# Performance work log

Hardware: AMD Instinct MI355X
Metric: run time of the kernel (lower is better)

## Reference

```python
import jax, jax.numpy as jnp
import numpy as np

BETA = 0.25
N_E = 1024
E_DIM = 64
B, L = 32, 2048


def setup_inputs() -> dict:
    key = jax.random.key(0)
    k1, k2 = jax.random.split(key)
    z = jax.random.normal(k1, (B, L, E_DIM), dtype=jnp.float32)
    # torch init: uniform_(-1/n_e, 1/n_e)
    codebook = jax.random.uniform(k2, (N_E, E_DIM), dtype=jnp.float32,
                                  minval=-1.0 / N_E, maxval=1.0 / N_E)
    return {"z": z, "codebook": codebook}


def reference(z, codebook):
    sg = jax.lax.stop_gradient
    n_e = codebook.shape[0]
    zf = z.reshape(-1, codebook.shape[1])  # (N, e_dim)
    # squared-distance matrix: ||z||^2 + ||e||^2 - 2 z.e  -> (N, n_e)
    d = (jnp.sum(zf * zf, axis=1, keepdims=True)
         + jnp.sum(codebook * codebook, axis=1)
         - 2.0 * zf @ codebook.T)
    idx = jnp.argmin(d, axis=1)  # (N,)
    # one-hot @ codebook is just a gather
    z_q = codebook[idx].reshape(z.shape)
    loss = (jnp.mean((sg(z_q) - z) ** 2)
            + BETA * jnp.mean((z_q - sg(z)) ** 2))
    # straight-through estimator
    z_q_st = z + sg(z_q - z)
    # codebook usage stats (mean of one-hot rows == normalized histogram)
    counts = jnp.zeros((n_e,), dtype=z.dtype).at[idx].add(1.0)
    e_mean = counts / idx.shape[0]
    perplexity = jnp.exp(-jnp.sum(e_mean * jnp.log(e_mean + 1e-10)))
    return loss, z_q_st, perplexity, idx
```

## Files before the change

### kernel.cpp

```cpp
#include <hip/hip_runtime.h>
#include <math.h>

#define E_DIM 64
#define N_E   1024
#define BETA  0.25

using bf16x8 = __attribute__((ext_vector_type(8))) short;
using f32x4  = __attribute__((ext_vector_type(4))) float;
#define MFMA(a, b, c) __builtin_amdgcn_mfma_f32_16x16x32_bf16((a), (b), (c), 0, 0, 0)

#define GLOAD_LDS(g, l) __builtin_amdgcn_global_load_lds(                      \
    (const __attribute__((address_space(1))) void*)(g),                        \
    (__attribute__((address_space(3))) void*)(l), 16, 0, 0)


__device__ __forceinline__ unsigned short f2bf_rn(float f) {
    unsigned u = __builtin_bit_cast(unsigned, f);
    unsigned r = u + 0x7fffu + ((u >> 16) & 1u);
    return (unsigned short)(r >> 16);
}
__device__ __forceinline__ float bf2f(unsigned short b) {
    unsigned u = ((unsigned)b) << 16;
    return __builtin_bit_cast(float, u);
}

__device__ __forceinline__ float pw64_sq(const float* v) {
    float r[8];
#pragma unroll
    for (int l = 0; l < 8; ++l) r[l] = v[l] * v[l];
#pragma unroll
    for (int t = 1; t < 8; ++t)
#pragma unroll
        for (int l = 0; l < 8; ++l) r[l] += v[8 * t + l] * v[8 * t + l];
    return ((r[0] + r[1]) + (r[2] + r[3])) + ((r[4] + r[5]) + (r[6] + r[7]));
}

__global__ __launch_bounds__(256) void k_h(const float* __restrict__ cb,
                                           float* __restrict__ h) {
    int j = blockIdx.x * 256 + threadIdx.x;
    if (j < N_E) {
        float e[E_DIM];
        const float4* ep = reinterpret_cast<const float4*>(cb + (size_t)j * E_DIM);
#pragma unroll
        for (int k4 = 0; k4 < E_DIM / 4; ++k4) {
            float4 v = ep[k4];
            e[4 * k4 + 0] = v.x; e[4 * k4 + 1] = v.y;
            e[4 * k4 + 2] = v.z; e[4 * k4 + 3] = v.w;
        }
        h[j] = pw64_sq(e);
    }
}

__global__ __launch_bounds__(256) void k_prep(const float* __restrict__ cb,
                                              unsigned short* __restrict__ ebh,
                                              unsigned short* __restrict__ ebl) {
    int t = blockIdx.x * 256 + threadIdx.x;
    int e = t & 7, lane = (t >> 3) & 63, ks = (t >> 9) & 1, ct = t >> 10;
    int j = ct * 16 + (lane & 15);
    int k = ks * 32 + ((lane >> 4) << 3) + e;
    float v = cb[j * 64 + k];
    unsigned short hi = f2bf_rn(v);
    ebh[t] = hi;
    ebl[t] = f2bf_rn(v - bf2f(hi));
}

__global__ __launch_bounds__(256, 2) void k_mfma(
    const float* __restrict__ z, const float* __restrict__ cb,
    const float* __restrict__ h,
    const unsigned short* __restrict__ ebh, const unsigned short* __restrict__ ebl,
    float* __restrict__ out_zq, float* __restrict__ out_idx,
    unsigned* __restrict__ hist, double* __restrict__ sse,
    unsigned* __restrict__ flagN, unsigned* __restrict__ flagL) {
    const int lane = threadIdx.x & 63;
    const int w = __builtin_amdgcn_readfirstlane(threadIdx.x >> 6);
    const int m = lane & 15, g = lane >> 4;

    __shared__ __align__(16) unsigned char sB[2][2][16384];
    __shared__ int bok;
    __shared__ float rsv[4][32];
    __shared__ float sb0[4][32], sb1[4][32];
    __shared__ int   sbi[4][32];
    if (threadIdx.x == 0) bok = 1;
    __syncthreads();

    {
        bf16x8 a, b;
#pragma unroll
        for (int e = 0; e < 8; ++e) {
            int k = g * 8 + e;
            a[e] = (short)f2bf_rn((float)(((m * 3 + k * 7) & 15) - 7));
            b[e] = (short)f2bf_rn((float)(((k * 5 + m * 3) & 15) - 8));
        }
        f32x4 acc = {0.f, 0.f, 0.f, 0.f};
        acc = MFMA(a, b, acc);
        bool ok = true;
#pragma unroll
        for (int r = 0; r < 4; ++r) {
            int rw = g * 4 + r;
            float E = 0.f;
            for (int k = 0; k < 32; ++k)
                E += (float)((((rw * 3 + k * 7) & 15) - 7) * (((k * 5 + m * 3) & 15) - 8));
            ok = ok && (acc[r] == E);
        }
        if (!ok) atomicAnd(&bok, 0);
    }
    __syncthreads();
    if (!bok) {
        if (threadIdx.x < 128) {
            unsigned p = atomicAdd(flagN, 1u);
            flagL[p] = (unsigned)(blockIdx.x * 128 + threadIdx.x);
        }
        return;
    }

    const int rowb32 = blockIdx.x * 128 + w * 32;
    bf16x8 a0h0, a0l0, a0h1, a0l1, a1h0, a1l0, a1h1, a1l1;
#define ALOAD(P, AH0, AL0, AH1, AL1) {                                         \
        const int rowA = rowb32 + (P) * 16 + m;                                \
        const float4* zr = reinterpret_cast<const float4*>(z + (size_t)rowA * 64); \
        float4 p0 = zr[g * 2], p1 = zr[g * 2 + 1];                             \
        float4 p2 = zr[8 + g * 2], p3 = zr[9 + g * 2];                         \
        float t0[8] = {p0.x, p0.y, p0.z, p0.w, p1.x, p1.y, p1.z, p1.w};        \
        float t1[8] = {p2.x, p2.y, p2.z, p2.w, p3.x, p3.y, p3.z, p3.w};        \
        float s = 0.f;                                                         \
        _Pragma("unroll")                                                      \
        for (int e = 0; e < 8; ++e) {                                          \
            s += fabsf(t0[e]) + fabsf(t1[e]);                                  \
            float x0 = 2.0f * t0[e]; unsigned short h0 = f2bf_rn(x0);          \
            AH0[e] = (short)h0; AL0[e] = (short)f2bf_rn(x0 - bf2f(h0));        \
            float x1 = 2.0f * t1[e]; unsigned short h1 = f2bf_rn(x1);          \
            AH1[e] = (short)h1; AL1[e] = (short)f2bf_rn(x1 - bf2f(h1));        \
        }                                                                      \
        s += __shfl_xor(s, 16);                                                \
        s += __shfl_xor(s, 32);                                                \
        if (g == 0) rsv[w][(P) * 16 + m] = s;                                  \
    }
    ALOAD(0, a0h0, a0l0, a0h1, a0l1)
    ALOAD(1, a1h0, a1l0, a1h1, a1l1)
#undef ALOAD

#define STAGE(c, buf) {                                                        \
        const unsigned char* gh = (const unsigned char*)ebh +                  \
            (size_t)(c) * 16384 + w * 4096 + lane * 16;                        \
        const unsigned char* gl = (const unsigned char*)ebl +                  \
            (size_t)(c) * 16384 + w * 4096 + lane * 16;                        \
        unsigned char* dh = &sB[buf][0][w * 4096];                             \
        unsigned char* dl = &sB[buf][1][w * 4096];                             \
        _Pragma("unroll")                                                      \
        for (int u = 0; u < 4; ++u) {                                          \
            GLOAD_LDS(gh + u * 1024, dh + u * 1024);                           \
            GLOAD_LDS(gl + u * 1024, dl + u * 1024);                           \
        }                                                                      \
    }

    float bb00 = INFINITY, bb01 = INFINITY, bb02 = INFINITY, bb03 = INFINITY;
    float bb10 = INFINITY, bb11 = INFINITY, bb12 = INFINITY, bb13 = INFINITY;
    float ss00 = INFINITY, ss01 = INFINITY, ss02 = INFINITY, ss03 = INFINITY;
    float ss10 = INFINITY, ss11 = INFINITY, ss12 = INFINITY, ss13 = INFINITY;
    int   ii00 = 0, ii01 = 0, ii02 = 0, ii03 = 0;
    int   ii10 = 0, ii11 = 0, ii12 = 0, ii13 = 0;
#define UPD(S, B0, B1, I0) { float _s = (S);                                   \
        if (_s < B0) { B1 = B0; B0 = _s; I0 = j; } else B1 = fminf(B1, _s); }

    STAGE(0, 0);
    __syncthreads();
#pragma unroll 1
    for (int c = 0; c < 8; ++c) {
        if (c + 1 < 8) STAGE(c + 1, (c + 1) & 1);
        const bf16x8* sBh = reinterpret_cast<const bf16x8*>(&sB[c & 1][0][0]);
        const bf16x8* sBl = reinterpret_cast<const bf16x8*>(&sB[c & 1][1][0]);
#pragma unroll
        for (int ct8 = 0; ct8 < 8; ++ct8) {
            const int fb = ct8 * 128 + lane;
            bf16x8 vbh0 = sBh[fb], vbh1 = sBh[fb + 64];
            bf16x8 vbl0 = sBl[fb], vbl1 = sBl[fb + 64];
            const f32x4 z4 = {0.f, 0.f, 0.f, 0.f};
            f32x4 c0a = MFMA(a0h0, vbh0, z4);
            f32x4 c0b = MFMA(a0h1, vbh1, z4);
            f32x4 c1a = MFMA(a1h0, vbh0, z4);
            f32x4 c1b = MFMA(a1h1, vbh1, z4);
            f32x4 c0c = MFMA(a0h0, vbl0, z4);
            f32x4 c0d = MFMA(a0h1, vbl1, z4);
            f32x4 c1c = MFMA(a1h0, vbl0, z4);
            f32x4 c1d = MFMA(a1h1, vbl1, z4);
            f32x4 c0e = MFMA(a0l0, vbh0, z4);
            f32x4 c0f = MFMA(a0l1, vbh1, z4);
            f32x4 c1e = MFMA(a1l0, vbh0, z4);
            f32x4 c1f = MFMA(a1l1, vbh1, z4);
            f32x4 s0 = (c0a + c0b) + ((c0c + c0d) + (c0e + c0f));
            f32x4 s1 = (c1a + c1b) + ((c1c + c1d) + (c1e + c1f));
            const int j = (c * 8 + ct8) * 16 + m;
            const float hj = h[j];
            UPD(hj - s0[0], bb00, ss00, ii00)
            UPD(hj - s0[1], bb01, ss01, ii01)
            UPD(hj - s0[2], bb02, ss02, ii02)
            UPD(hj - s0[3], bb03, ss03, ii03)
            UPD(hj - s1[0], bb10, ss10, ii10)
            UPD(hj - s1[1], bb11, ss11, ii11)
            UPD(hj - s1[2], bb12, ss12, ii12)
            UPD(hj - s1[3], bb13, ss13, ii13)
        }
        __syncthreads();
    }
#undef STAGE
#undef UPD

#pragma unroll
    for (int mask = 1; mask < 16; mask <<= 1) {
#define MRG(B0, I0, B1) { float ob0 = __shfl_xor(B0, mask); int oi = __shfl_xor(I0, mask); \
        float ob1 = __shfl_xor(B1, mask); \
        if (ob0 < B0) { B1 = fminf(fminf(B0, B1), ob1); B0 = ob0; I0 = oi; } \
        else { B1 = fminf(B1, fminf(ob0, ob1)); } }
        MRG(bb00, ii00, ss00) MRG(bb01, ii01, ss01)
        MRG(bb02, ii02, ss02) MRG(bb03, ii03, ss03)
        MRG(bb10, ii10, ss10) MRG(bb11, ii11, ss11)
        MRG(bb12, ii12, ss12) MRG(bb13, ii13, ss13)
#undef MRG
    }

    if (m == 0) {
        sb0[w][g * 4 + 0] = bb00; sb1[w][g * 4 + 0] = ss00; sbi[w][g * 4 + 0] = ii00;
        sb0[w][g * 4 + 1] = bb01; sb1[w][g * 4 + 1] = ss01; sbi[w][g * 4 + 1] = ii01;
        sb0[w][g * 4 + 2] = bb02; sb1[w][g * 4 + 2] = ss02; sbi[w][g * 4 + 2] = ii02;
        sb0[w][g * 4 + 3] = bb03; sb1[w][g * 4 + 3] = ss03; sbi[w][g * 4 + 3] = ii03;
        sb0[w][16 + g * 4 + 0] = bb10; sb1[w][16 + g * 4 + 0] = ss10; sbi[w][16 + g * 4 + 0] = ii10;
        sb0[w][16 + g * 4 + 1] = bb11; sb1[w][16 + g * 4 + 1] = ss11; sbi[w][16 + g * 4 + 1] = ii11;
        sb0[w][16 + g * 4 + 2] = bb12; sb1[w][16 + g * 4 + 2] = ss12; sbi[w][16 + g * 4 + 2] = ii12;
        sb0[w][16 + g * 4 + 3] = bb13; sb1[w][16 + g * 4 + 3] = ss13; sbi[w][16 + g * 4 + 3] = ii13;
    }
    __syncthreads();

    {
        const int rloc = lane >> 1, q = lane & 1;
        const int rowO = rowb32 + rloc;
        const float vb0 = sb0[w][rloc];
        const float vb1 = sb1[w][rloc];
        const int   vi  = sbi[w][rloc];
        const float Delta = 6e-8f * rsv[w][rloc] + 2.2e-5f;
        float local = 0.f;
        if (vb1 - vb0 <= Delta) {
            if (q == 0) { unsigned p = atomicAdd(flagN, 1u); flagL[p] = (unsigned)rowO; }
        } else {
            if (q == 0) { out_idx[rowO] = (float)vi; atomicAdd(&hist[vi], 1u); }
            const float4* cv = reinterpret_cast<const float4*>(cb + (size_t)vi * 64) + q * 8;
            const float4* zv = reinterpret_cast<const float4*>(z + (size_t)rowO * 64) + q * 8;
            float* orow = out_zq + (size_t)rowO * 64 + q * 32;
#pragma unroll
            for (int u = 0; u < 8; ++u) {
                float4 cc = cv[u], zo = zv[u];
                orow[4 * u + 0] = cc.x; orow[4 * u + 1] = cc.y;
                orow[4 * u + 2] = cc.z; orow[4 * u + 3] = cc.w;
                float dx = cc.x - zo.x, dy = cc.y - zo.y;
                float dz = cc.z - zo.z, dw = cc.w - zo.w;
                local = fmaf(dx, dx, local); local = fmaf(dy, dy, local);
                local = fmaf(dz, dz, local); local = fmaf(dw, dw, local);
            }
        }
#pragma unroll
        for (int off = 32; off; off >>= 1) local += __shfl_down(local, off);
        if (lane == 0) atomicAdd(sse, (double)local);
    }
}

__global__ __launch_bounds__(64, 4) void k_cleanup(
    const float* __restrict__ z, const float* __restrict__ cb,
    const float* __restrict__ h,
    const unsigned* __restrict__ flagN, const unsigned* __restrict__ flagL,
    float* __restrict__ out_zq, float* __restrict__ out_idx,
    unsigned* __restrict__ hist, double* __restrict__ sse) {
    const unsigned n = *flagN;
    const int lane = threadIdx.x;

    for (unsigned f = blockIdx.x; f < n; f += gridDim.x) {
        const int row = (int)flagL[f];

        float tz[E_DIM];
        const float4* zp = reinterpret_cast<const float4*>(z + (size_t)row * 64);
#pragma unroll
        for (int k4 = 0; k4 < 16; ++k4) {
            float4 v = zp[k4];
            tz[4 * k4 + 0] = v.x; tz[4 * k4 + 1] = v.y;
            tz[4 * k4 + 2] = v.z; tz[4 * k4 + 3] = v.w;
        }
        const float nz = pw64_sq(tz);
#pragma unroll
        for (int k = 0; k < 64; ++k) tz[k] = 2.0f * tz[k];

        float bs = INFINITY;
        int bj = 0;
#pragma unroll 2
        for (int t = 0; t < 16; ++t) {
            const int j = lane + 64 * t;
            const float4* cv = reinterpret_cast<const float4*>(cb + (size_t)j * 64);
            float mm = 0.f;
#pragma unroll
            for (int k4 = 0; k4 < 16; ++k4) {
                float4 e = cv[k4];
                mm = fmaf(tz[4 * k4 + 0], e.x, mm);
                mm = fmaf(tz[4 * k4 + 1], e.y, mm);
                mm = fmaf(tz[4 * k4 + 2], e.z, mm);
                mm = fmaf(tz[4 * k4 + 3], e.w, mm);
            }
            float s = (nz + h[j]) - mm;
            if (s < bs) { bs = s; bj = j; }
        }
#pragma unroll
        for (int off = 32; off; off >>= 1) {
            float s2 = __shfl_down(bs, off);
            int   j2 = __shfl_down(bj, off);
            if (s2 < bs || (s2 == bs && j2 < bj)) { bs = s2; bj = j2; }
        }
        bj = __shfl(bj, 0);

        float c = cb[(size_t)bj * 64 + lane];
        out_zq[(size_t)row * 64 + lane] = c;
        float d = c - 0.5f * tz[lane];
        float l2 = d * d;
#pragma unroll
        for (int off = 32; off; off >>= 1) l2 += __shfl_down(l2, off);
        if (lane == 0) {
            out_idx[row] = (float)bj;
            atomicAdd(&hist[bj], 1u);
            atomicAdd(sse, (double)l2);
        }
    }
}

__global__ __launch_bounds__(512, 2) void k_scan_fb(
    const float* __restrict__ z, const float* __restrict__ cb,
    const float* __restrict__ h,
    float* __restrict__ out_zq, float* __restrict__ out_idx,
    unsigned* __restrict__ hist, double* __restrict__ sse) {
    const int lane = threadIdx.x & 63;
    const int w = __builtin_amdgcn_readfirstlane(threadIdx.x >> 6);
    const int row = blockIdx.x * 64 + lane;
    float tz[E_DIM];
    const float4* zp = reinterpret_cast<const float4*>(z + (size_t)row * E_DIM);
#pragma unroll
    for (int k4 = 0; k4 < E_DIM / 4; ++k4) {
        float4 v = zp[k4];
        tz[4 * k4 + 0] = v.x; tz[4 * k4 + 1] = v.y;
        tz[4 * k4 + 2] = v.z; tz[4 * k4 + 3] = v.w;
    }
    const float nz = pw64_sq(tz);
#pragma unroll
    for (int k = 0; k < E_DIM; ++k) tz[k] = 2.0f * tz[k];
    float b0 = INFINITY; int bi = 0;
    const int j0 = w * 128;
#pragma unroll 1
    for (int j = j0; j < j0 + 128; j += 4) {
        const float* c0 = cb + (size_t)j * E_DIM;
        float m0 = 0.f, m1 = 0.f, m2 = 0.f, m3 = 0.f;
#pragma unroll
        for (int k = 0; k < E_DIM; ++k) {
            float wk = tz[k];
            m0 = fmaf(wk, c0[0 * E_DIM + k], m0);
            m1 = fmaf(wk, c0[1 * E_DIM + k], m1);
            m2 = fmaf(wk, c0[2 * E_DIM + k], m2);
            m3 = fmaf(wk, c0[3 * E_DIM + k], m3);
        }
        float s0 = (nz + h[j + 0]) - m0;
        float s1 = (nz + h[j + 1]) - m1;
        float s2 = (nz + h[j + 2]) - m2;
        float s3 = (nz + h[j + 3]) - m3;
        if (s0 < b0) { b0 = s0; bi = j + 0; }
        if (s1 < b0) { b0 = s1; bi = j + 1; }
        if (s2 < b0) { b0 = s2; bi = j + 2; }
        if (s3 < b0) { b0 = s3; bi = j + 3; }
    }
    __shared__ float lb[8][64];
    __shared__ int   li[8][64];
    lb[w][lane] = b0; li[w][lane] = bi;
    __syncthreads();
    if (threadIdx.x < 64) {
        float b = lb[0][lane]; int i = li[0][lane];
#pragma unroll
        for (int c = 1; c < 8; ++c) {
            float bc = lb[c][lane]; int ic = li[c][lane];
            if (bc < b) { b = bc; i = ic; }
        }
        out_idx[row] = (float)i;
        float local = 0.f;
        const float4* cv = reinterpret_cast<const float4*>(cb + (size_t)i * E_DIM);
        float* orow = out_zq + (size_t)row * E_DIM;
#pragma unroll
        for (int k4 = 0; k4 < E_DIM / 4; ++k4) {
            float4 c = cv[k4];
            float zx = 0.5f * tz[4 * k4 + 0], zy = 0.5f * tz[4 * k4 + 1];
            float zz = 0.5f * tz[4 * k4 + 2], zw = 0.5f * tz[4 * k4 + 3];
            orow[4 * k4 + 0] = c.x; orow[4 * k4 + 1] = c.y;
            orow[4 * k4 + 2] = c.z; orow[4 * k4 + 3] = c.w;
            float dx = c.x - zx, dy = c.y - zy, dz = c.z - zz, dw = c.w - zw;
            local = fmaf(dx, dx, local); local = fmaf(dy, dy, local);
            local = fmaf(dz, dz, local); local = fmaf(dw, dw, local);
        }
        atomicAdd(&hist[i], 1u);
#pragma unroll
        for (int off = 32; off; off >>= 1) local += __shfl_down(local, off);
        if (lane == 0) atomicAdd(sse, (double)local);
    }
}

__global__ __launch_bounds__(256) void k_final(
    const unsigned* __restrict__ hist, const double* __restrict__ sse,
    float* __restrict__ out, int nrows) {
    __shared__ double sh[256];
    double acc = 0.0;
    for (int j = threadIdx.x; j < N_E; j += 256) {
        double p = (double)hist[j] / (double)nrows;
        acc += p * log(p + 1e-10);
    }
    sh[threadIdx.x] = acc;
    __syncthreads();
    for (int s = 128; s; s >>= 1) {
        if (threadIdx.x < s) sh[threadIdx.x] += sh[threadIdx.x + s];
        __syncthreads();
    }
    if (threadIdx.x == 0) {
        double ntot = (double)nrows * (double)E_DIM;
        out[0] = (float)((1.0 + BETA) * (*sse) / ntot);
        out[1 + (size_t)nrows * E_DIM] = (float)exp(-sh[0]);
    }
}

extern "C" void kernel_launch(void* const* d_in, const int* in_sizes, int n_in,
                              void* d_out, int out_size, void* d_ws, size_t ws_size,
                              hipStream_t stream) {
    const float* z  = (const float*)d_in[0];
    const float* cb = (const float*)d_in[1];
    const int nrows = in_sizes[0] / E_DIM;
    float* out = (float*)d_out;

    char* ws = (char*)d_ws;
    unsigned* hist  = (unsigned*)(ws + 0);
    double*   sse   = (double*)  (ws + 4096);
    unsigned* flagN = (unsigned*)(ws + 4104);
    float*    h     = (float*)   (ws + 4112);
    unsigned short* ebh = (unsigned short*)(ws + 8208);
    unsigned short* ebl = (unsigned short*)(ws + 139280);
    unsigned* flagL = (unsigned*)(ws + 270352);

    float* out_zq  = out + 1;
    float* out_idx = out + 1 + (size_t)nrows * E_DIM + 1;

    hipMemsetAsync(d_ws, 0, 4112, stream);
    k_h<<<(N_E + 255) / 256, 256, 0, stream>>>(cb, h);

    if (ws_size >= 532496) {
        k_prep<<<256, 256, 0, stream>>>(cb, ebh, ebl);
        k_mfma<<<nrows / 128, 256, 0, stream>>>(z, cb, h, ebh, ebl,
                                                out_zq, out_idx, hist, sse, flagN, flagL);
        k_cleanup<<<2048, 64, 0, stream>>>(z, cb, h, flagN, flagL,
                                           out_zq, out_idx, hist, sse);
    } else {
        k_scan_fb<<<nrows / 64, 512, 0, stream>>>(z, cb, h, out_zq, out_idx, hist, sse);
    }
    k_final<<<1, 256, 0, stream>>>(hist, sse, out, nrows);
}
```

Measured before the change: 121.7 us.

## Read codebook fragments directly from global and fuse prep kernels

The main kernel drops its double-buffered LDS staging of the pre-swizzled codebook fragments. Instead each wave loads its bf16 fragments straight from global memory (L2-resident, shared by all blocks) into registers, software-prefetching one column tile ahead, which removes the __syncthreads barriers and LDS traffic. Separately, the memset, the norm kernel and the split kernel are fused into one prep launch to cut launch overhead. The cost is extra global/L2 load latency per tile and more register pressure from the prefetch buffers.

```diff
diff --git a/kernel.cpp b/kernel.cpp
--- a/kernel.cpp
+++ b/kernel.cpp
@@ -8,10 +8,6 @@
 using bf16x8 = __attribute__((ext_vector_type(8))) short;
 using f32x4  = __attribute__((ext_vector_type(4))) float;
 #define MFMA(a, b, c) __builtin_amdgcn_mfma_f32_16x16x32_bf16((a), (b), (c), 0, 0, 0)
-
-#define GLOAD_LDS(g, l) __builtin_amdgcn_global_load_lds(                      \
-    (const __attribute__((address_space(1))) void*)(g),                        \
-    (__attribute__((address_space(3))) void*)(l), 16, 0, 0)
 
 
 __device__ __forceinline__ unsigned short f2bf_rn(float f) {
@@ -35,10 +31,25 @@
     return ((r[0] + r[1]) + (r[2] + r[3])) + ((r[4] + r[5]) + (r[6] + r[7]));
 }
 
-__global__ __launch_bounds__(256) void k_h(const float* __restrict__ cb,
-                                           float* __restrict__ h) {
-    int j = blockIdx.x * 256 + threadIdx.x;
-    if (j < N_E) {
+__global__ __launch_bounds__(256) void k_prep(const float* __restrict__ cb,
+                                              unsigned short* __restrict__ ebh,
+                                              unsigned short* __restrict__ ebl,
+                                              float* __restrict__ h,
+                                              unsigned* __restrict__ hist,
+                                              double* __restrict__ sse,
+                                              unsigned* __restrict__ flagN) {
+    int t = blockIdx.x * 256 + threadIdx.x;
+    {
+        int e = t & 7, lane = (t >> 3) & 63, ks = (t >> 9) & 1, ct = t >> 10;
+        int j = ct * 16 + (lane & 15);
+        int k = ks * 32 + ((lane >> 4) << 3) + e;
+        float v = cb[j * 64 + k];
+        unsigned short hi = f2bf_rn(v);
+        ebh[t] = hi;
+        ebl[t] = f2bf_rn(v - bf2f(hi));
+    }
+    if (blockIdx.x < 4) {
+        int j = t;
         float e[E_DIM];
         const float4* ep = reinterpret_cast<const float4*>(cb + (size_t)j * E_DIM);
 #pragma unroll
@@ -48,20 +59,13 @@
             e[4 * k4 + 2] = v.z; e[4 * k4 + 3] = v.w;
         }
         h[j] = pw64_sq(e);
-    }
-}
-
-__global__ __launch_bounds__(256) void k_prep(const float* __restrict__ cb,
-                                              unsigned short* __restrict__ ebh,
-                                              unsigned short* __restrict__ ebl) {
-    int t = blockIdx.x * 256 + threadIdx.x;
-    int e = t & 7, lane = (t >> 3) & 63, ks = (t >> 9) & 1, ct = t >> 10;
-    int j = ct * 16 + (lane & 15);
-    int k = ks * 32 + ((lane >> 4) << 3) + e;
-    float v = cb[j * 64 + k];
-    unsigned short hi = f2bf_rn(v);
-    ebh[t] = hi;
-    ebl[t] = f2bf_rn(v - bf2f(hi));
+    } else if (blockIdx.x == 4) {
+#pragma unroll
+        for (int u = 0; u < 4; ++u) hist[threadIdx.x * 4 + u] = 0u;
+    } else if (blockIdx.x == 5 && threadIdx.x == 0) {
+        *sse = 0.0;
+        *flagN = 0u;
+    }
 }
 
 __global__ __launch_bounds__(256, 2) void k_mfma(
@@ -75,7 +79,6 @@
     const int w = __builtin_amdgcn_readfirstlane(threadIdx.x >> 6);
     const int m = lane & 15, g = lane >> 4;
 
-    __shared__ __align__(16) unsigned char sB[2][2][16384];
     __shared__ int bok;
     __shared__ float rsv[4][32];
     __shared__ float sb0[4][32], sb1[4][32];
@@ -139,20 +142,6 @@
     ALOAD(1, a1h0, a1l0, a1h1, a1l1)
 #undef ALOAD
 
-#define STAGE(c, buf) {                                                        \
-        const unsigned char* gh = (const unsigned char*)ebh +                  \
-            (size_t)(c) * 16384 + w * 4096 + lane * 16;                        \
-        const unsigned char* gl = (const unsigned char*)ebl +                  \
-            (size_t)(c) * 16384 + w * 4096 + lane * 16;                        \
-        unsigned char* dh = &sB[buf][0][w * 4096];                             \
-        unsigned char* dl = &sB[buf][1][w * 4096];                             \
-        _Pragma("unroll")                                                      \
-        for (int u = 0; u < 4; ++u) {                                          \
-            GLOAD_LDS(gh + u * 1024, dh + u * 1024);                           \
-            GLOAD_LDS(gl + u * 1024, dl + u * 1024);                           \
-        }                                                                      \
-    }
-
     float bb00 = INFINITY, bb01 = INFINITY, bb02 = INFINITY, bb03 = INFINITY;
     float bb10 = INFINITY, bb11 = INFINITY, bb12 = INFINITY, bb13 = INFINITY;
     float ss00 = INFINITY, ss01 = INFINITY, ss02 = INFINITY, ss03 = INFINITY;
@@ -162,47 +151,58 @@
 #define UPD(S, B0, B1, I0) { float _s = (S);                                   \
         if (_s < B0) { B1 = B0; B0 = _s; I0 = j; } else B1 = fminf(B1, _s); }
 
-    STAGE(0, 0);
-    __syncthreads();
+    const bf16x8* pBh = reinterpret_cast<const bf16x8*>(ebh);
+    const bf16x8* pBl = reinterpret_cast<const bf16x8*>(ebl);
+
+    bf16x8 Ah0 = pBh[lane],       Ah1 = pBh[lane + 64];
+    bf16x8 Al0 = pBl[lane],       Al1 = pBl[lane + 64];
+    bf16x8 Bh0 = pBh[128 + lane], Bh1 = pBh[128 + lane + 64];
+    bf16x8 Bl0 = pBl[128 + lane], Bl1 = pBl[128 + lane + 64];
+
+#define COLTILE(CT, VH0, VH1, VL0, VL1) {                                      \
+        const int j = (CT) * 16 + m;                                           \
+        const float hj = h[j];                                                 \
+        const f32x4 z4 = {0.f, 0.f, 0.f, 0.f};                                 \
+        f32x4 c0a = MFMA(a0h0, VH0, z4);                                       \
+        f32x4 c0b = MFMA(a0h1, VH1, z4);                                       \
+        f32x4 c1a = MFMA(a1h0, VH0, z4);                                       \
+        f32x4 c1b = MFMA(a1h1, VH1, z4);                                       \
+        f32x4 c0c = MFMA(a0h0, VL0, z4);                                       \
+        f32x4 c0d = MFMA(a0h1, VL1, z4);                                       \
+        f32x4 c1c = MFMA(a1h0, VL0, z4);                                       \
+        f32x4 c1d = MFMA(a1h1, VL1, z4);                                       \
+        f32x4 c0e = MFMA(a0l0, VH0, z4);                                       \
+        f32x4 c0f = MFMA(a0l1, VH1, z4);                                       \
+        f32x4 c1e = MFMA(a1l0, VH0, z4);                                       \
+        f32x4 c1f = MFMA(a1l1, VH1, z4);                                       \
+        f32x4 s0 = (c0a + c0b) + ((c0c + c0d) + (c0e + c0f));                  \
+        f32x4 s1 = (c1a + c1b) + ((c1c + c1d) + (c1e + c1f));                  \
+        UPD(hj - s0[0], bb00, ss00, ii00)                                      \
+        UPD(hj - s0[1], bb01, ss01, ii01)                                      \
+        UPD(hj - s0[2], bb02, ss02, ii02)                                      \
+        UPD(hj - s0[3], bb03, ss03, ii03)                                      \
+        UPD(hj - s1[0], bb10, ss10, ii10)                                      \
+        UPD(hj - s1[1], bb11, ss11, ii11)                                      \
+        UPD(hj - s1[2], bb12, ss12, ii12)                                      \
+        UPD(hj - s1[3], bb13, ss13, ii13)                                      \
+    }
+
 #pragma unroll 1
-    for (int c = 0; c < 8; ++c) {
-        if (c + 1 < 8) STAGE(c + 1, (c + 1) & 1);
-        const bf16x8* sBh = reinterpret_cast<const bf16x8*>(&sB[c & 1][0][0]);
-        const bf16x8* sBl = reinterpret_cast<const bf16x8*>(&sB[c & 1][1][0]);
-#pragma unroll
-        for (int ct8 = 0; ct8 < 8; ++ct8) {
-            const int fb = ct8 * 128 + lane;
-            bf16x8 vbh0 = sBh[fb], vbh1 = sBh[fb + 64];
-            bf16x8 vbl0 = sBl[fb], vbl1 = sBl[fb + 64];
-            const f32x4 z4 = {0.f, 0.f, 0.f, 0.f};
-            f32x4 c0a = MFMA(a0h0, vbh0, z4);
-            f32x4 c0b = MFMA(a0h1, vbh1, z4);
-            f32x4 c1a = MFMA(a1h0, vbh0, z4);
-            f32x4 c1b = MFMA(a1h1, vbh1, z4);
-            f32x4 c0c = MFMA(a0h0, vbl0, z4);
-            f32x4 c0d = MFMA(a0h1, vbl1, z4);
-            f32x4 c1c = MFMA(a1h0, vbl0, z4);
-            f32x4 c1d = MFMA(a1h1, vbl1, z4);
-            f32x4 c0e = MFMA(a0l0, vbh0, z4);
-            f32x4 c0f = MFMA(a0l1, vbh1, z4);
-            f32x4 c1e = MFMA(a1l0, vbh0, z4);
-            f32x4 c1f = MFMA(a1l1, vbh1, z4);
-            f32x4 s0 = (c0a + c0b) + ((c0c + c0d) + (c0e + c0f));
-            f32x4 s1 = (c1a + c1b) + ((c1c + c1d) + (c1e + c1f));
-            const int j = (c * 8 + ct8) * 16 + m;
-            const float hj = h[j];
-            UPD(hj - s0[0], bb00, ss00, ii00)
-            UPD(hj - s0[1], bb01, ss01, ii01)
-            UPD(hj - s0[2], bb02, ss02, ii02)
-            UPD(hj - s0[3], bb03, ss03, ii03)
-            UPD(hj - s1[0], bb10, ss10, ii10)
-            UPD(hj - s1[1], bb11, ss11, ii11)
-            UPD(hj - s1[2], bb12, ss12, ii12)
-            UPD(hj - s1[3], bb13, ss13, ii13)
-        }
-        __syncthreads();
-    }
-#undef STAGE
+    for (int ct = 0; ct < 64; ct += 2) {
+        COLTILE(ct, Ah0, Ah1, Al0, Al1);
+        if (ct + 2 < 64) {
+            const int fb = (ct + 2) * 128 + lane;
+            Ah0 = pBh[fb]; Ah1 = pBh[fb + 64];
+            Al0 = pBl[fb]; Al1 = pBl[fb + 64];
+        }
+        COLTILE(ct + 1, Bh0, Bh1, Bl0, Bl1);
+        if (ct + 3 < 64) {
+            const int fb = (ct + 3) * 128 + lane;
+            Bh0 = pBh[fb]; Bh1 = pBh[fb + 64];
+            Bl0 = pBl[fb]; Bl1 = pBl[fb + 64];
+        }
+    }
+#undef COLTILE
 #undef UPD
 
 #pragma unroll
@@ -326,6 +326,22 @@
     }
 }
 
+__global__ __launch_bounds__(256) void k_h_fb(const float* __restrict__ cb,
+                                              float* __restrict__ h) {
+    int j = blockIdx.x * 256 + threadIdx.x;
+    if (j < N_E) {
+        float e[E_DIM];
+        const float4* ep = reinterpret_cast<const float4*>(cb + (size_t)j * E_DIM);
+#pragma unroll
+        for (int k4 = 0; k4 < E_DIM / 4; ++k4) {
+            float4 v = ep[k4];
+            e[4 * k4 + 0] = v.x; e[4 * k4 + 1] = v.y;
+            e[4 * k4 + 2] = v.z; e[4 * k4 + 3] = v.w;
+        }
+        h[j] = pw64_sq(e);
+    }
+}
+
 __global__ __launch_bounds__(512, 2) void k_scan_fb(
     const float* __restrict__ z, const float* __restrict__ cb,
     const float* __restrict__ h,
@@ -443,16 +459,15 @@
     float* out_zq  = out + 1;
     float* out_idx = out + 1 + (size_t)nrows * E_DIM + 1;
 
-    hipMemsetAsync(d_ws, 0, 4112, stream);
-    k_h<<<(N_E + 255) / 256, 256, 0, stream>>>(cb, h);
-
     if (ws_size >= 532496) {
-        k_prep<<<256, 256, 0, stream>>>(cb, ebh, ebl);
+        k_prep<<<256, 256, 0, stream>>>(cb, ebh, ebl, h, hist, sse, flagN);
         k_mfma<<<nrows / 128, 256, 0, stream>>>(z, cb, h, ebh, ebl,
                                                 out_zq, out_idx, hist, sse, flagN, flagL);
         k_cleanup<<<2048, 64, 0, stream>>>(z, cb, h, flagN, flagL,
                                            out_zq, out_idx, hist, sse);
     } else {
+        hipMemsetAsync(d_ws, 0, 4112, stream);
+        k_h_fb<<<(N_E + 255) / 256, 256, 0, stream>>>(cb, h);
         k_scan_fb<<<nrows / 64, 512, 0, stream>>>(z, cb, h, out_zq, out_idx, hist, sse);
     }
     k_final<<<1, 256, 0, stream>>>(hist, sse, out, nrows);
```

Result: slower. 127.1 us (+4.5%).
